# Kernel optimization log

Measured on AMD Instinct MI355X. Metric: run time of the kernel, lower is better.

Reference implementation:

```python
import jax, jax.numpy as jnp
import numpy as np

B, NUM_GENES, F = 8, 20000, 128
N, E, H = 50000, 800000, 128


def setup_inputs() -> dict:
    key = jax.random.key(0)
    k = jax.random.split(key, 8)
    gene_emb = jax.random.normal(k[0], (B, NUM_GENES, F), dtype=jnp.float32)
    W1 = jax.random.normal(k[1], (F, H), dtype=jnp.float32) * 0.05
    b1 = jnp.zeros((H,), dtype=jnp.float32)
    W2 = jax.random.normal(k[2], (H, H), dtype=jnp.float32) * 0.05
    b2 = jnp.zeros((H,), dtype=jnp.float32)
    global_ids = jax.random.randint(k[3], (N,), 0, NUM_GENES, dtype=jnp.int64)
    edge_index = jax.random.randint(k[4], (2, E), 0, N, dtype=jnp.int64)
    return {"gene_emb": gene_emb, "W1": W1, "b1": b1, "W2": W2, "b2": b2,
            "global_ids": global_ids, "edge_index": edge_index}


def reference(gene_emb, W1, b1, W2, b2, global_ids, edge_index):
    n = global_ids.shape[0]
    # GCN normalization with self-loops (PyG GCNConv default):
    # A_hat = A + I, deg over target nodes, norm = d^{-1/2}[src] * d^{-1/2}[dst]
    loop = jnp.arange(n)
    src = jnp.concatenate([edge_index[0], loop])  # [E+N]
    dst = jnp.concatenate([edge_index[1], loop])  # [E+N]
    deg = jnp.zeros((n,), gene_emb.dtype).at[dst].add(1.0)
    dinv = jax.lax.rsqrt(deg)  # deg >= 1 thanks to self-loops
    norm = (dinv[src] * dinv[dst])[None, :, None]  # [1, E+N, 1]

    def gcn(x, W, b):
        h = x @ W                                   # [B, N, H] transform first (linear commutes)
        msg = h[:, src, :] * norm                   # gather + scale: [B, E+N, H]
        agg = jnp.zeros_like(h).at[:, dst].add(msg)  # scatter-add over targets
        return agg + b

    x = gene_emb[:, global_ids, :]                  # [B, N, F] node feature gather
    x = jax.nn.relu(gcn(x, W1, b1))
    x = gcn(x, W2, b2)
    # global_mean_pool: each batch replica is one whole graph -> mean over nodes
    return x.mean(axis=1)                           # [B, H]
```

## Files before the change

### kernel.cpp

```cpp
#include <hip/hip_runtime.h>

#define NG 20000
#define BB 8
#define FD 128

typedef unsigned int uint;
typedef unsigned short ushort;
typedef __attribute__((ext_vector_type(8))) short short8v;
typedef __attribute__((ext_vector_type(4))) float float4v;
typedef __attribute__((ext_vector_type(4))) int int4v;
typedef __attribute__((ext_vector_type(2))) float f2v;

__device__ f2v llvm_rbl_v2f32(int4v srsrc, int voffset, int soffset, int aux)
    __asm("llvm.amdgcn.raw.buffer.load.v2f32");

__device__ __forceinline__ int4v make_srsrc(const void* p) {
    int4v r;
    r.x = (int)(uint)(uintptr_t)p;
    r.y = (int)(uint)((uintptr_t)p >> 32);
    r.z = -1;
    r.w = 0x00020000;
    return r;
}

__device__ __forceinline__ ushort f2bf(float x) {
    uint u = __float_as_uint(x);
    u += 0x7FFFu + ((u >> 16) & 1u);
    return (ushort)(u >> 16);
}
__device__ __forceinline__ float bf_lo(uint u) { return __uint_as_float(u << 16); }
__device__ __forceinline__ float bf_hi(uint u) { return __uint_as_float(u & 0xFFFF0000u); }

__global__ void k_setup(int* ideg, float* s_acc,
                        const float* __restrict__ W1, ushort* w1t, int N) {
    int i = blockIdx.x * blockDim.x + threadIdx.x;
    if (i < N) ideg[i] = 0;
    if (i < 8 * BB * FD) s_acc[i] = 0.0f;
    if (i < FD * FD) {
        int j = i >> 7, k = i & 127;
        w1t[i] = f2bf(W1[k * 128 + j]);
    }
}

__global__ void k_count(const int* __restrict__ dst, int* ideg, int E) {
    int e = blockIdx.x * blockDim.x + threadIdx.x;
    if (e < E) atomicAdd(&ideg[dst[e]], 1);
}

__global__ void k_scanA(const int* __restrict__ ideg, float* dinv, float* cval,
                        int* padcnt, int* offs, int* bsums, int N) {
    __shared__ int sd[256];
    int t = threadIdx.x, idx = blockIdx.x * 256 + t;
    int v = 0;
    if (idx < N) {
        int d = ideg[idx] + 1;
        float fd = (float)d;
        dinv[idx] = rsqrtf(fd);
        cval[idx] = 1.0f / fd;
        v = (d + 7) & ~7;
        padcnt[idx] = v;
    }
    sd[t] = v; __syncthreads();
    for (int o = 1; o < 256; o <<= 1) {
        int x = (t >= o) ? sd[t - o] : 0;
        __syncthreads();
        sd[t] += x;
        __syncthreads();
    }
    if (idx < N) offs[idx] = sd[t] - v;
    if (t == 255) bsums[blockIdx.x] = sd[255];
}

__global__ void k_scanB(int* offs, const int* __restrict__ bsums,
                        const int* __restrict__ ideg, const int* __restrict__ padcnt,
                        const int* __restrict__ gid,
                        int* cursor, int2* csr, int N, int nb) {
    __shared__ int sd[256];
    int t = threadIdx.x;
    int v = (t < nb) ? bsums[t] : 0;
    sd[t] = v; __syncthreads();
    for (int o = 1; o < 256; o <<= 1) {
        int x = (t >= o) ? sd[t - o] : 0;
        __syncthreads();
        sd[t] += x;
        __syncthreads();
    }
    int bid = blockIdx.x;
    int prefix = (bid > 0) ? sd[bid - 1] : 0;
    int i = bid * 256 + t;
    if (i < N) {
        int o = offs[i] + prefix;
        offs[i] = o;
        int d  = ideg[i] + 1;
        int v8 = padcnt[i];
        float iv = 1.0f / (float)d;
        csr[o] = make_int2(gid[i], __float_as_int(iv));
        cursor[i] = 1;
        for (int z = d; z < v8; z++) csr[o + z] = make_int2(0, 0);
    }
}

__global__ __launch_bounds__(256, 3)
void k_fillh(const int* __restrict__ src, const int* __restrict__ dst,
             const int* __restrict__ gid, const float* __restrict__ dinv,
             float* cval, const int* __restrict__ offs, int* cursor,
             int2* csr, int E, int eb,
             const float* __restrict__ gene, const ushort* __restrict__ w1t,
             uint* __restrict__ h2u) {
    __shared__ __align__(16) char smem[49152];
    if ((int)blockIdx.x < eb) {
        int e = blockIdx.x * 256 + threadIdx.x;
        if (e >= E) return;
        int s = src[e], d = dst[e];
        float nrm = dinv[s] * dinv[d];
        atomicAdd(&cval[s], nrm);
        int pos = atomicAdd(&cursor[d], 1);
        csr[offs[d] + pos] = make_int2(gid[s], __float_as_int(nrm));
        return;
    }
    ushort* Al = (ushort*)smem;
    ushort* Bl = (ushort*)(smem + 16384);
    float*  Cl = (float*)smem;
    int t = threadIdx.x;
    int hb   = blockIdx.x - eb;
    int p    = hb & 3;
    int tile = hb >> 2;
    int g0   = tile * 32;

#pragma unroll
    for (int s = 0; s < 8; s++) {
        int f = t + s * 256;
        int r = f >> 5, k0 = (f & 31) * 4;
        int bb = 2 * p + (r >> 5);
        int gg = g0 + (r & 31);
        float4 v = *(const float4*)(gene + ((size_t)bb * NG + gg) * 128 + k0);
        ushort4 u;
        u.x = f2bf(v.x); u.y = f2bf(v.y); u.z = f2bf(v.z); u.w = f2bf(v.w);
        int byte = (r * 256 + k0 * 2) ^ ((r & 7) << 4);
        *(ushort4*)((char*)Al + byte) = u;
    }
#pragma unroll
    for (int s = 0; s < 8; s++) {
        int f = t + s * 256;
        int j = f >> 4, k0 = (f & 15) * 8;
        uint4 v = *(const uint4*)(w1t + j * 128 + k0);
        int byte = (j * 256 + k0 * 2) ^ ((j & 7) << 4);
        *(uint4*)((char*)Bl + byte) = v;
    }
    __syncthreads();

    int wid = t >> 6, lane = t & 63;
    int r0 = wid * 16;
    int lrow = lane & 15, lhi = lane >> 4;
    float4v acc[8];
#pragma unroll
    for (int nf = 0; nf < 8; nf++) acc[nf] = (float4v)(0.f);

#pragma unroll
    for (int c = 0; c < 4; c++) {
        int ra = r0 + lrow;
        int byteA = (ra * 256 + (c * 32 + lhi * 8) * 2) ^ ((ra & 7) << 4);
        short8v a = *(short8v*)((char*)Al + byteA);
#pragma unroll
        for (int nf = 0; nf < 8; nf++) {
            int jb = nf * 16 + lrow;
            int byteB = (jb * 256 + (c * 32 + lhi * 8) * 2) ^ ((jb & 7) << 4);
            short8v b = *(short8v*)((char*)Bl + byteB);
            acc[nf] = __builtin_amdgcn_mfma_f32_16x16x32_bf16(a, b, acc[nf], 0, 0, 0);
        }
    }
    __syncthreads();

#pragma unroll
    for (int nf = 0; nf < 8; nf++) {
#pragma unroll
        for (int q = 0; q < 4; q++) {
            Cl[(r0 + lhi * 4 + q) * 128 + nf * 16 + lrow] = acc[nf][q];
        }
    }
    __syncthreads();

#pragma unroll
    for (int s = 0; s < 16; s++) {
        int flat = t + s * 256;
        int gi = flat >> 7, cc = flat & 127;
        float lo = Cl[gi * 128 + cc];
        float hi = Cl[(32 + gi) * 128 + cc];
        uint u = (uint)f2bf(lo) | ((uint)f2bf(hi) << 16);
        h2u[((size_t)p * NG + g0 + gi) * 128 + cc] = u;
    }
}

__global__ __launch_bounds__(512)
void k_aggp(const uint* __restrict__ hp, const int2* __restrict__ csr,
            const int* __restrict__ offs, const int* __restrict__ padcnt,
            const float* __restrict__ cval, const float* __restrict__ b1,
            float* __restrict__ s_acc, int N, int wpp) {
    int p    = blockIdx.x & 3;
    int wid  = threadIdx.x >> 6, lane = threadIdx.x & 63;
    int w    = __builtin_amdgcn_readfirstlane((blockIdx.x >> 2) * 8 + wid);
    int4v sr = make_srsrc(hp + (size_t)p * NG * 128);
    int voff = lane * 8;
    int l2 = lane * 2;
    float bx = b1[l2], by = b1[l2 + 1];
    float sx0 = 0.f, sx1 = 0.f, sy0 = 0.f, sy1 = 0.f;

    int i0 = (int)((long long)w * N / wpp);
    int i1 = (int)((long long)(w + 1) * N / wpp);
    for (int i = i0; i < i1; ++i) {
        int   e  = offs[i];
        int   pc = padcnt[i];
        float cv = cval[i];
        float ax0 = 0.f, ax1 = 0.f, ay0 = 0.f, ay1 = 0.f;
        for (int q = 0; q < pc; q += 8) {
            int ee = e + q;
            int2 c0 = csr[ee],     c1 = csr[ee + 1], c2 = csr[ee + 2], c3 = csr[ee + 3];
            int2 c4 = csr[ee + 4], c5 = csr[ee + 5], c6 = csr[ee + 6], c7 = csr[ee + 7];
            f2v u0 = llvm_rbl_v2f32(sr, voff, c0.x << 9, 0);
            f2v u1 = llvm_rbl_v2f32(sr, voff, c1.x << 9, 0);
            f2v u2 = llvm_rbl_v2f32(sr, voff, c2.x << 9, 0);
            f2v u3 = llvm_rbl_v2f32(sr, voff, c3.x << 9, 0);
            f2v u4 = llvm_rbl_v2f32(sr, voff, c4.x << 9, 0);
            f2v u5 = llvm_rbl_v2f32(sr, voff, c5.x << 9, 0);
            f2v u6 = llvm_rbl_v2f32(sr, voff, c6.x << 9, 0);
            f2v u7 = llvm_rbl_v2f32(sr, voff, c7.x << 9, 0);
            float n0 = __int_as_float(c0.y), n1 = __int_as_float(c1.y);
            float n2 = __int_as_float(c2.y), n3 = __int_as_float(c3.y);
            float n4 = __int_as_float(c4.y), n5 = __int_as_float(c5.y);
            float n6 = __int_as_float(c6.y), n7 = __int_as_float(c7.y);
            uint a, b;
            a = __float_as_uint(u0.x); b = __float_as_uint(u0.y);
            ax0 = fmaf(n0, bf_lo(a), ax0); ax1 = fmaf(n0, bf_hi(a), ax1);
            ay0 = fmaf(n0, bf_lo(b), ay0); ay1 = fmaf(n0, bf_hi(b), ay1);
            a = __float_as_uint(u1.x); b = __float_as_uint(u1.y);
            ax0 = fmaf(n1, bf_lo(a), ax0); ax1 = fmaf(n1, bf_hi(a), ax1);
            ay0 = fmaf(n1, bf_lo(b), ay0); ay1 = fmaf(n1, bf_hi(b), ay1);
            a = __float_as_uint(u2.x); b = __float_as_uint(u2.y);
            ax0 = fmaf(n2, bf_lo(a), ax0); ax1 = fmaf(n2, bf_hi(a), ax1);
            ay0 = fmaf(n2, bf_lo(b), ay0); ay1 = fmaf(n2, bf_hi(b), ay1);
            a = __float_as_uint(u3.x); b = __float_as_uint(u3.y);
            ax0 = fmaf(n3, bf_lo(a), ax0); ax1 = fmaf(n3, bf_hi(a), ax1);
            ay0 = fmaf(n3, bf_lo(b), ay0); ay1 = fmaf(n3, bf_hi(b), ay1);
            a = __float_as_uint(u4.x); b = __float_as_uint(u4.y);
            ax0 = fmaf(n4, bf_lo(a), ax0); ax1 = fmaf(n4, bf_hi(a), ax1);
            ay0 = fmaf(n4, bf_lo(b), ay0); ay1 = fmaf(n4, bf_hi(b), ay1);
            a = __float_as_uint(u5.x); b = __float_as_uint(u5.y);
            ax0 = fmaf(n5, bf_lo(a), ax0); ax1 = fmaf(n5, bf_hi(a), ax1);
            ay0 = fmaf(n5, bf_lo(b), ay0); ay1 = fmaf(n5, bf_hi(b), ay1);
            a = __float_as_uint(u6.x); b = __float_as_uint(u6.y);
            ax0 = fmaf(n6, bf_lo(a), ax0); ax1 = fmaf(n6, bf_hi(a), ax1);
            ay0 = fmaf(n6, bf_lo(b), ay0); ay1 = fmaf(n6, bf_hi(b), ay1);
            a = __float_as_uint(u7.x); b = __float_as_uint(u7.y);
            ax0 = fmaf(n7, bf_lo(a), ax0); ax1 = fmaf(n7, bf_hi(a), ax1);
            ay0 = fmaf(n7, bf_lo(b), ay0); ay1 = fmaf(n7, bf_hi(b), ay1);
        }
        sx0 += cv * fmaxf(ax0 + bx, 0.f);
        sx1 += cv * fmaxf(ax1 + bx, 0.f);
        sy0 += cv * fmaxf(ay0 + by, 0.f);
        sy1 += cv * fmaxf(ay1 + by, 0.f);
    }

    __shared__ float red[8][256];
    red[wid][lane * 4 + 0] = sx0;
    red[wid][lane * 4 + 1] = sx1;
    red[wid][lane * 4 + 2] = sy0;
    red[wid][lane * 4 + 3] = sy1;
    __syncthreads();
    int t = threadIdx.x;
    if (t < 256) {
        float s = 0.f;
#pragma unroll
        for (int wv = 0; wv < 8; wv++) s += red[wv][t];
        int l = t >> 2, c = t & 3;
        int rep = (blockIdx.x >> 2) & 7;
        atomicAdd(&s_acc[rep * 1024 + (2 * p + (c & 1)) * 128 + 2 * l + (c >> 1)], s);
    }
}

__global__ void k_final(const float* __restrict__ s_acc, const float* __restrict__ W2,
                        const float* __restrict__ b2, float* __restrict__ out, float invN) {
    __shared__ float ss[1024];
    int t = threadIdx.x;
    for (int idx = t; idx < 1024; idx += 128) {
        float s = 0.f;
#pragma unroll
        for (int r = 0; r < 8; r++) s += s_acc[r * 1024 + idx];
        ss[idx] = s;
    }
    __syncthreads();
    float acc[8];
#pragma unroll
    for (int b = 0; b < 8; b++) acc[b] = 0.f;
    for (int k = 0; k < 128; k++) {
        float w = W2[k * 128 + t];
#pragma unroll
        for (int b = 0; b < 8; b++) acc[b] += ss[b * 128 + k] * w;
    }
    float bb = b2[t];
#pragma unroll
    for (int b = 0; b < 8; b++) out[b * 128 + t] = acc[b] * invN + bb;
}


extern "C" void kernel_launch(void* const* d_in, const int* in_sizes, int n_in,
                              void* d_out, int out_size, void* d_ws, size_t ws_size,
                              hipStream_t stream) {
    const float* gene = (const float*)d_in[0];
    const float* W1   = (const float*)d_in[1];
    const float* b1   = (const float*)d_in[2];
    const float* W2   = (const float*)d_in[3];
    const float* b2   = (const float*)d_in[4];
    const int*   gid  = (const int*)d_in[5];
    const int*   eidx = (const int*)d_in[6];
    int N = in_sizes[5];
    int E = in_sizes[6] / 2;
    const int* src = eidx;
    const int* dst = eidx + E;
    float* out = (float*)d_out;

    char* p = (char*)d_ws;
    auto alloc = [&](size_t bytes) -> char* {
        char* r = p; p += (bytes + 255) & ~(size_t)255; return r;
    };
    size_t csr_cap = (size_t)E + 8 * (size_t)N;
    int*   ideg   = (int*)  alloc((size_t)N * 4);
    float* dinv   = (float*)alloc((size_t)N * 4);
    float* cval   = (float*)alloc((size_t)N * 4);
    int*   padcnt = (int*)  alloc((size_t)N * 4);
    int*   offs   = (int*)  alloc((size_t)N * 4);
    int*   cursor = (int*)  alloc((size_t)N * 4);
    int*   bsums  = (int*)  alloc(256 * 4);
    int2*  csr    = (int2*) alloc(csr_cap * 8);
    float* s_acc  = (float*)alloc(8 * 1024 * 4);
    uint*  h2     = (uint*) alloc((size_t)NG * BB * FD * 2);
    ushort* w1t   = (ushort*)alloc(128 * 128 * 2);

    int nb = (N + 255) / 256;
    int eb = (E + 255) / 256;
    int hblk = 4 * (NG / 32);

    const int NBLK = 2048;
    int wpp = (NBLK / 4) * 8;

    k_setup<<<nb, 256, 0, stream>>>(ideg, s_acc, W1, w1t, N);
    k_count<<<eb, 256, 0, stream>>>(dst, ideg, E);
    k_scanA<<<nb, 256, 0, stream>>>(ideg, dinv, cval, padcnt, offs, bsums, N);
    k_scanB<<<nb, 256, 0, stream>>>(offs, bsums, ideg, padcnt, gid, cursor, csr, N, nb);
    k_fillh<<<eb + hblk, 256, 0, stream>>>(src, dst, gid, dinv, cval, offs, cursor,
                                           csr, E, eb, gene, w1t, h2);
    k_aggp <<<NBLK, 512, 0, stream>>>(h2, csr, offs, padcnt,
                                      cval, b1, s_acc, N, wpp);
    k_final<<<1, 128, 0, stream>>>(s_acc, W2, b2, out, 1.0f / (float)N);
}
```

Before: 304.0 us.

## Split gene transform across count and fill kernels, merge scans with atomic ticket

Moves the gene-embedding MFMA transform into a shared helper. Half the tiles now run inside the degree-count kernel and the other half stay in the CSR-fill kernel, so the atomic-heavy edge passes overlap with matmul work. The two-pass prefix scan becomes a single kernel in which each block takes its base offset from a global atomic ticket. That drops one launch but gives the CSR segments an order that depends on block scheduling. This is still correct because offs is stored per node.

Result: no change. 305.9 us (+0.6%).

```diff
diff --git a/kernel.cpp b/kernel.cpp
--- a/kernel.cpp
+++ b/kernel.cpp
@@ -3,6 +3,7 @@
 #define NG 20000
 #define BB 8
 #define FD 128
+#define H1 1250
 
 typedef unsigned int uint;
 typedef unsigned short ushort;
@@ -31,32 +32,119 @@
 __device__ __forceinline__ float bf_lo(uint u) { return __uint_as_float(u << 16); }
 __device__ __forceinline__ float bf_hi(uint u) { return __uint_as_float(u & 0xFFFF0000u); }
 
-__global__ void k_setup(int* ideg, float* s_acc,
+__device__ __forceinline__ void h_tile(char* smem, int hb,
+                                       const float* __restrict__ gene,
+                                       const ushort* __restrict__ w1t,
+                                       uint* __restrict__ h2u, int t) {
+    ushort* Al = (ushort*)smem;
+    ushort* Bl = (ushort*)(smem + 16384);
+    float*  Cl = (float*)smem;
+    int p  = hb & 3;
+    int g0 = (hb >> 2) * 32;
+
+#pragma unroll
+    for (int s = 0; s < 8; s++) {
+        int f = t + s * 256;
+        int r = f >> 5, k0 = (f & 31) * 4;
+        int bb = 2 * p + (r >> 5);
+        int gg = g0 + (r & 31);
+        float4 v = *(const float4*)(gene + ((size_t)bb * NG + gg) * 128 + k0);
+        ushort4 u;
+        u.x = f2bf(v.x); u.y = f2bf(v.y); u.z = f2bf(v.z); u.w = f2bf(v.w);
+        int byte = (r * 256 + k0 * 2) ^ ((r & 7) << 4);
+        *(ushort4*)(smem + byte) = u;
+    }
+#pragma unroll
+    for (int s = 0; s < 8; s++) {
+        int f = t + s * 256;
+        int j = f >> 4, k0 = (f & 15) * 8;
+        uint4 v = *(const uint4*)(w1t + j * 128 + k0);
+        int byte = (j * 256 + k0 * 2) ^ ((j & 7) << 4);
+        *(uint4*)((char*)Bl + byte) = v;
+    }
+    __syncthreads();
+
+    int wid = t >> 6, lane = t & 63;
+    int r0 = wid * 16;
+    int lrow = lane & 15, lhi = lane >> 4;
+    float4v acc[8];
+#pragma unroll
+    for (int nf = 0; nf < 8; nf++) acc[nf] = (float4v)(0.f);
+
+#pragma unroll
+    for (int c = 0; c < 4; c++) {
+        int ra = r0 + lrow;
+        int byteA = (ra * 256 + (c * 32 + lhi * 8) * 2) ^ ((ra & 7) << 4);
+        short8v a = *(short8v*)((char*)Al + byteA);
+#pragma unroll
+        for (int nf = 0; nf < 8; nf++) {
+            int jb = nf * 16 + lrow;
+            int byteB = (jb * 256 + (c * 32 + lhi * 8) * 2) ^ ((jb & 7) << 4);
+            short8v b = *(short8v*)((char*)Bl + byteB);
+            acc[nf] = __builtin_amdgcn_mfma_f32_16x16x32_bf16(a, b, acc[nf], 0, 0, 0);
+        }
+    }
+    __syncthreads();
+
+#pragma unroll
+    for (int nf = 0; nf < 8; nf++) {
+#pragma unroll
+        for (int q = 0; q < 4; q++) {
+            Cl[(r0 + lhi * 4 + q) * 128 + nf * 16 + lrow] = acc[nf][q];
+        }
+    }
+    __syncthreads();
+
+#pragma unroll
+    for (int s = 0; s < 16; s++) {
+        int flat = t + s * 256;
+        int gi = flat >> 7, cc = flat & 127;
+        float lo = Cl[gi * 128 + cc];
+        float hi = Cl[(32 + gi) * 128 + cc];
+        uint u = (uint)f2bf(lo) | ((uint)f2bf(hi) << 16);
+        h2u[((size_t)p * NG + g0 + gi) * 128 + cc] = u;
+    }
+}
+
+__global__ void k_setup(int* ideg, float* s_acc, int* ticket,
                         const float* __restrict__ W1, ushort* w1t, int N) {
     int i = blockIdx.x * blockDim.x + threadIdx.x;
     if (i < N) ideg[i] = 0;
     if (i < 8 * BB * FD) s_acc[i] = 0.0f;
+    if (i == 0) *ticket = 0;
     if (i < FD * FD) {
         int j = i >> 7, k = i & 127;
         w1t[i] = f2bf(W1[k * 128 + j]);
     }
 }
 
-__global__ void k_count(const int* __restrict__ dst, int* ideg, int E) {
-    int e = blockIdx.x * blockDim.x + threadIdx.x;
-    if (e < E) atomicAdd(&ideg[dst[e]], 1);
-}
-
-__global__ void k_scanA(const int* __restrict__ ideg, float* dinv, float* cval,
-                        int* padcnt, int* offs, int* bsums, int N) {
+__global__ __launch_bounds__(256, 3)
+void k_counth(const int* __restrict__ dst, int* ideg, int E, int eb,
+              const float* __restrict__ gene, const ushort* __restrict__ w1t,
+              uint* __restrict__ h2u) {
+    __shared__ __align__(16) char smem[49152];
+    if ((int)blockIdx.x < eb) {
+        int e = blockIdx.x * 256 + threadIdx.x;
+        if (e < E) atomicAdd(&ideg[dst[e]], 1);
+        return;
+    }
+    h_tile(smem, blockIdx.x - eb, gene, w1t, h2u, threadIdx.x);
+}
+
+__global__ void k_scan(const int* __restrict__ ideg, float* dinv, float* cval,
+                       int* padcnt, int* offs, const int* __restrict__ gid,
+                       int* cursor, int2* csr, int* ticket, int N) {
     __shared__ int sd[256];
+    __shared__ int sbase;
     int t = threadIdx.x, idx = blockIdx.x * 256 + t;
-    int v = 0;
+    int v = 0, d = 0;
+    float iv = 0.f;
     if (idx < N) {
-        int d = ideg[idx] + 1;
+        d = ideg[idx] + 1;
         float fd = (float)d;
         dinv[idx] = rsqrtf(fd);
-        cval[idx] = 1.0f / fd;
+        iv = 1.0f / fd;
+        cval[idx] = iv;
         v = (d + 7) & ~7;
         padcnt[idx] = v;
     }
@@ -67,36 +155,14 @@
         sd[t] += x;
         __syncthreads();
     }
-    if (idx < N) offs[idx] = sd[t] - v;
-    if (t == 255) bsums[blockIdx.x] = sd[255];
-}
-
-__global__ void k_scanB(int* offs, const int* __restrict__ bsums,
-                        const int* __restrict__ ideg, const int* __restrict__ padcnt,
-                        const int* __restrict__ gid,
-                        int* cursor, int2* csr, int N, int nb) {
-    __shared__ int sd[256];
-    int t = threadIdx.x;
-    int v = (t < nb) ? bsums[t] : 0;
-    sd[t] = v; __syncthreads();
-    for (int o = 1; o < 256; o <<= 1) {
-        int x = (t >= o) ? sd[t - o] : 0;
-        __syncthreads();
-        sd[t] += x;
-        __syncthreads();
-    }
-    int bid = blockIdx.x;
-    int prefix = (bid > 0) ? sd[bid - 1] : 0;
-    int i = bid * 256 + t;
-    if (i < N) {
-        int o = offs[i] + prefix;
-        offs[i] = o;
-        int d  = ideg[i] + 1;
-        int v8 = padcnt[i];
-        float iv = 1.0f / (float)d;
-        csr[o] = make_int2(gid[i], __float_as_int(iv));
-        cursor[i] = 1;
-        for (int z = d; z < v8; z++) csr[o + z] = make_int2(0, 0);
+    if (t == 255) sbase = atomicAdd(ticket, sd[255]);
+    __syncthreads();
+    if (idx < N) {
+        int o = sbase + sd[t] - v;
+        offs[idx] = o;
+        csr[o] = make_int2(gid[idx], __float_as_int(iv));
+        cursor[idx] = 1;
+        for (int z = d; z < v; z++) csr[o + z] = make_int2(0, 0);
     }
 }
 
@@ -118,77 +184,7 @@
         csr[offs[d] + pos] = make_int2(gid[s], __float_as_int(nrm));
         return;
     }
-    ushort* Al = (ushort*)smem;
-    ushort* Bl = (ushort*)(smem + 16384);
-    float*  Cl = (float*)smem;
-    int t = threadIdx.x;
-    int hb   = blockIdx.x - eb;
-    int p    = hb & 3;
-    int tile = hb >> 2;
-    int g0   = tile * 32;
-
-#pragma unroll
-    for (int s = 0; s < 8; s++) {
-        int f = t + s * 256;
-        int r = f >> 5, k0 = (f & 31) * 4;
-        int bb = 2 * p + (r >> 5);
-        int gg = g0 + (r & 31);
-        float4 v = *(const float4*)(gene + ((size_t)bb * NG + gg) * 128 + k0);
-        ushort4 u;
-        u.x = f2bf(v.x); u.y = f2bf(v.y); u.z = f2bf(v.z); u.w = f2bf(v.w);
-        int byte = (r * 256 + k0 * 2) ^ ((r & 7) << 4);
-        *(ushort4*)((char*)Al + byte) = u;
-    }
-#pragma unroll
-    for (int s = 0; s < 8; s++) {
-        int f = t + s * 256;
-        int j = f >> 4, k0 = (f & 15) * 8;
-        uint4 v = *(const uint4*)(w1t + j * 128 + k0);
-        int byte = (j * 256 + k0 * 2) ^ ((j & 7) << 4);
-        *(uint4*)((char*)Bl + byte) = v;
-    }
-    __syncthreads();
-
-    int wid = t >> 6, lane = t & 63;
-    int r0 = wid * 16;
-    int lrow = lane & 15, lhi = lane >> 4;
-    float4v acc[8];
-#pragma unroll
-    for (int nf = 0; nf < 8; nf++) acc[nf] = (float4v)(0.f);
-
-#pragma unroll
-    for (int c = 0; c < 4; c++) {
-        int ra = r0 + lrow;
-        int byteA = (ra * 256 + (c * 32 + lhi * 8) * 2) ^ ((ra & 7) << 4);
-        short8v a = *(short8v*)((char*)Al + byteA);
-#pragma unroll
-        for (int nf = 0; nf < 8; nf++) {
-            int jb = nf * 16 + lrow;
-            int byteB = (jb * 256 + (c * 32 + lhi * 8) * 2) ^ ((jb & 7) << 4);
-            short8v b = *(short8v*)((char*)Bl + byteB);
-            acc[nf] = __builtin_amdgcn_mfma_f32_16x16x32_bf16(a, b, acc[nf], 0, 0, 0);
-        }
-    }
-    __syncthreads();
-
-#pragma unroll
-    for (int nf = 0; nf < 8; nf++) {
-#pragma unroll
-        for (int q = 0; q < 4; q++) {
-            Cl[(r0 + lhi * 4 + q) * 128 + nf * 16 + lrow] = acc[nf][q];
-        }
-    }
-    __syncthreads();
-
-#pragma unroll
-    for (int s = 0; s < 16; s++) {
-        int flat = t + s * 256;
-        int gi = flat >> 7, cc = flat & 127;
-        float lo = Cl[gi * 128 + cc];
-        float hi = Cl[(32 + gi) * 128 + cc];
-        uint u = (uint)f2bf(lo) | ((uint)f2bf(hi) << 16);
-        h2u[((size_t)p * NG + g0 + gi) * 128 + cc] = u;
-    }
+    h_tile(smem, (int)blockIdx.x - eb + H1, gene, w1t, h2u, threadIdx.x);
 }
 
 __global__ __launch_bounds__(512)
@@ -329,7 +325,7 @@
     int*   padcnt = (int*)  alloc((size_t)N * 4);
     int*   offs   = (int*)  alloc((size_t)N * 4);
     int*   cursor = (int*)  alloc((size_t)N * 4);
-    int*   bsums  = (int*)  alloc(256 * 4);
+    int*   ticket = (int*)  alloc(256);
     int2*  csr    = (int2*) alloc(csr_cap * 8);
     float* s_acc  = (float*)alloc(8 * 1024 * 4);
     uint*  h2     = (uint*) alloc((size_t)NG * BB * FD * 2);
@@ -342,13 +338,13 @@
     const int NBLK = 2048;
     int wpp = (NBLK / 4) * 8;
 
-    k_setup<<<nb, 256, 0, stream>>>(ideg, s_acc, W1, w1t, N);
-    k_count<<<eb, 256, 0, stream>>>(dst, ideg, E);
-    k_scanA<<<nb, 256, 0, stream>>>(ideg, dinv, cval, padcnt, offs, bsums, N);
-    k_scanB<<<nb, 256, 0, stream>>>(offs, bsums, ideg, padcnt, gid, cursor, csr, N, nb);
-    k_fillh<<<eb + hblk, 256, 0, stream>>>(src, dst, gid, dinv, cval, offs, cursor,
-                                           csr, E, eb, gene, w1t, h2);
-    k_aggp <<<NBLK, 512, 0, stream>>>(h2, csr, offs, padcnt,
-                                      cval, b1, s_acc, N, wpp);
-    k_final<<<1, 128, 0, stream>>>(s_acc, W2, b2, out, 1.0f / (float)N);
-}
+    k_setup <<<nb, 256, 0, stream>>>(ideg, s_acc, ticket, W1, w1t, N);
+    k_counth<<<eb + H1, 256, 0, stream>>>(dst, ideg, E, eb, gene, w1t, h2);
+    k_scan  <<<nb, 256, 0, stream>>>(ideg, dinv, cval, padcnt, offs, gid,
+                                     cursor, csr, ticket, N);
+    k_fillh <<<eb + (hblk - H1), 256, 0, stream>>>(src, dst, gid, dinv, cval, offs,
+                                                   cursor, csr, E, eb, gene, w1t, h2);
+    k_aggp  <<<NBLK, 512, 0, stream>>>(h2, csr, offs, padcnt,
+                                       cval, b1, s_acc, N, wpp);
+    k_final <<<1, 128, 0, stream>>>(s_acc, W2, b2, out, 1.0f / (float)N);
+}
```
